# Performance work log

Measured on AMD Instinct MI355X. Metric: run time of the kernel, lower is better.

Reference implementation:

```python
import jax, jax.numpy as jnp
import numpy as np

B, N, E = 16, 1024, 256
H, D = 16, 16            # head_num * qkv_dim == embedding_dim
FF = 2 * E               # ff_size = embedding_dim * 2
EPS = 1e-5


def setup_inputs() -> dict:
    key = jax.random.key(0)
    ks = jax.random.split(key, 12)
    s = lambda fan_in: 1.0 / np.sqrt(fan_in)
    return {
        "x":  jax.random.normal(ks[0], (B, N, E), dtype=jnp.float32),
        # attention projections (nn.Linear, bias=False) stored as [in, out]
        "Wq": jax.random.uniform(ks[1], (E, H * D), jnp.float32, -s(E), s(E)),
        "Wk": jax.random.uniform(ks[2], (E, H * D), jnp.float32, -s(E), s(E)),
        "Wv": jax.random.uniform(ks[3], (E, H * D), jnp.float32, -s(E), s(E)),
        "Wo": jax.random.uniform(ks[4], (H * D, E), jnp.float32, -s(H * D), s(H * D)),
        "bo": jax.random.uniform(ks[5], (E,), jnp.float32, -s(H * D), s(H * D)),
        # InstanceNorm1d affine params
        "gamma1": jnp.ones((E,), jnp.float32),
        "beta1":  jnp.zeros((E,), jnp.float32),
        "gamma2": jnp.ones((E,), jnp.float32),
        "beta2":  jnp.zeros((E,), jnp.float32),
        # SwiGLU FFN: Linear(E, 2*FF) -> SwiGLU -> Linear(FF, E)
        "W1": jax.random.uniform(ks[6], (E, 2 * FF), jnp.float32, -s(E), s(E)),
        "b1": jax.random.uniform(ks[7], (2 * FF,), jnp.float32, -s(E), s(E)),
        "W2": jax.random.uniform(ks[8], (FF, E), jnp.float32, -s(FF), s(FF)),
        "b2": jax.random.uniform(ks[9], (E,), jnp.float32, -s(FF), s(FF)),
    }


def _instance_norm(x, gamma, beta):
    # x: [B, N, E]; normalize over N per (batch, channel), biased variance
    mean = jnp.mean(x, axis=1, keepdims=True)
    var = jnp.mean(jnp.square(x - mean), axis=1, keepdims=True)
    return (x - mean) * jax.lax.rsqrt(var + EPS) * gamma + beta


def reference(x, Wq, Wk, Wv, Wo, bo, gamma1, beta1, gamma2, beta2, W1, b1, W2, b2):
    b, n, e = x.shape
    q = (x @ Wq).reshape(b, n, H, D)
    k = (x @ Wk).reshape(b, n, H, D)
    v = (x @ Wv).reshape(b, n, H, D)
    scores = jnp.einsum("bnhd,bmhd->bhnm", q, k) / np.sqrt(D)   # [B,H,N,N]
    weights = jax.nn.softmax(scores, axis=-1)
    attn = jnp.einsum("bhnm,bmhd->bnhd", weights, v).reshape(b, n, H * D)
    mha = attn @ Wo + bo
    h = _instance_norm(mha + x, gamma1, beta1)
    # SwiGLU FFN: chunk -> (x_part, gate); silu(gate) * x_part
    proj = h @ W1 + b1
    x_part, gate = proj[..., :FF], proj[..., FF:]
    ff = (jax.nn.silu(gate) * x_part) @ W2 + b2
    return _instance_norm(h + ff, gamma2, beta2)
```

## Files before the change

kernel.cpp:

```cpp
#include <hip/hip_runtime.h>
#include <stdint.h>

typedef unsigned short u16;
typedef __bf16 bf16x8 __attribute__((ext_vector_type(8)));
typedef float f32x4 __attribute__((ext_vector_type(4)));

__device__ __forceinline__ float bf2f(u16 v){ return __uint_as_float(((unsigned)v)<<16); }
__device__ __forceinline__ u16 f2bf(float f){
  unsigned u = __float_as_uint(f);
  unsigned r = (u + 0x7FFFu + ((u>>16)&1u)) >> 16;
  return (u16)r;
}
__device__ __forceinline__ float fexp2(float x){
#if __has_builtin(__builtin_amdgcn_exp2f)
  return __builtin_amdgcn_exp2f(x);
#else
  return exp2f(x);
#endif
}

__global__ void prep_kernel(const float* __restrict__ x_, u16* __restrict__ xb,
                            const float* __restrict__ Wq, const float* __restrict__ Wk,
                            const float* __restrict__ Wv, const float* __restrict__ Wo,
                            const float* __restrict__ W1, const float* __restrict__ W2,
                            u16* __restrict__ wqkvT, u16* __restrict__ woT,
                            u16* __restrict__ w1T, u16* __restrict__ w2T)
{
  int bid = blockIdx.x;
  int t = threadIdx.x;
  if (bid >= 640) {
    int idx = ((bid - 640) * 256 + t) * 8;
    float4 a0 = *(const float4*)(x_ + idx);
    float4 a1 = *(const float4*)(x_ + idx + 4);
    union { u16 u[8]; uint4 v; } pk;
    pk.u[0] = f2bf(a0.x); pk.u[1] = f2bf(a0.y); pk.u[2] = f2bf(a0.z); pk.u[3] = f2bf(a0.w);
    pk.u[4] = f2bf(a1.x); pk.u[5] = f2bf(a1.y); pk.u[6] = f2bf(a1.z); pk.u[7] = f2bf(a1.w);
    *(uint4*)(xb + idx) = pk.v;
    return;
  }
  __shared__ u16 tile[32][33];
  const float* in; u16* out; int K, N, t2; bool glu = false;
  if (bid < 64)       { in = Wq; out = wqkvT;           K = 256; N = 256;  t2 = bid; }
  else if (bid < 128) { in = Wk; out = wqkvT + 65536;   K = 256; N = 256;  t2 = bid - 64; }
  else if (bid < 192) { in = Wv; out = wqkvT + 131072;  K = 256; N = 256;  t2 = bid - 128; }
  else if (bid < 256) { in = Wo; out = woT;             K = 256; N = 256;  t2 = bid - 192; }
  else if (bid < 512) { in = W1; out = w1T;             K = 256; N = 1024; t2 = bid - 256; glu = true; }
  else                { in = W2; out = w2T;             K = 512; N = 256;  t2 = bid - 512; }
  int ntn = N >> 5;
  int k0 = (t2 / ntn) * 32, n0 = (t2 % ntn) * 32;
  #pragma unroll
  for (int p = 0; p < 4; ++p) {
    int u = t + p * 256; int r = u >> 5, c = u & 31;
    tile[r][c] = f2bf(in[(size_t)(k0 + r) * N + n0 + c]);
  }
  __syncthreads();
  #pragma unroll
  for (int p = 0; p < 4; ++p) {
    int u = t + p * 256; int r = u >> 5, c = u & 31;
    int q = n0 + r;
    int row = glu ? (q < 512 ? 2 * q : 2 * (q - 512) + 1) : q;
    out[(size_t)row * K + k0 + c] = tile[c][r];
  }
}

enum { MODE_QKV = 0, MODE_Y_RES = 1, MODE_GLU = 2 };

template<int MODE, int RESF32, int STATS>
__launch_bounds__(256, 2)
__global__ void gemm_kernel(const u16* __restrict__ A, const u16* __restrict__ BT,
                            int M, int N, int K,
                            const float* __restrict__ bias, const void* __restrict__ resp,
                            u16* __restrict__ outB,
                            float* __restrict__ ssum, float* __restrict__ ssq)
{
  __shared__ u16 As[128 * 40];
  __shared__ u16 Bs[128 * 40];
  const int t = threadIdx.x;
  const int m0 = blockIdx.x * 128;
  const int n0 = blockIdx.y * 128;
  const int lane = t & 63;
  const int w = t >> 6;
  const int wm = (w >> 1) * 64;
  const int wn = (w & 1) * 64;
  const int fr = lane & 15;
  const int fg = lane >> 4;

  f32x4 acc[4][4];
  #pragma unroll
  for (int i = 0; i < 4; ++i)
    #pragma unroll
    for (int j = 0; j < 4; ++j)
      acc[i][j] = (f32x4){0.f, 0.f, 0.f, 0.f};

  for (int k0 = 0; k0 < K; k0 += 32) {
    __syncthreads();
    #pragma unroll
    for (int p = 0; p < 2; ++p) {
      int u = t + p * 256;
      int row = u >> 2, cb = u & 3;
      float4 va = *(const float4*)(A + (size_t)(m0 + row) * K + k0 + cb * 8);
      *(float4*)(As + row * 40 + cb * 8) = va;
      float4 vb = *(const float4*)(BT + (size_t)(n0 + row) * K + k0 + cb * 8);
      *(float4*)(Bs + row * 40 + cb * 8) = vb;
    }
    __syncthreads();
    bf16x8 af[4], bfr[4];
    #pragma unroll
    for (int i = 0; i < 4; ++i) af[i]  = *(const bf16x8*)(As + (wm + i * 16 + fr) * 40 + fg * 8);
    #pragma unroll
    for (int j = 0; j < 4; ++j) bfr[j] = *(const bf16x8*)(Bs + (wn + j * 16 + fr) * 40 + fg * 8);
    #pragma unroll
    for (int i = 0; i < 4; ++i)
      #pragma unroll
      for (int j = 0; j < 4; ++j)
        acc[i][j] = __builtin_amdgcn_mfma_f32_16x16x32_bf16(af[i], bfr[j], acc[i][j], 0, 0, 0);
  }

  const int bIdx = m0 >> 10;
  #pragma unroll
  for (int j = 0; j < 4; ++j) {
    int col = n0 + wn + j * 16 + fr;
    float bv = 0.f;
    if (MODE == MODE_Y_RES) bv = bias[col];
    if (MODE == MODE_GLU)   bv = bias[(col >> 1) + ((col & 1) << 9)];
    float sj = 0.f, qj = 0.f;
    #pragma unroll
    for (int i = 0; i < 4; ++i) {
      #pragma unroll
      for (int r = 0; r < 4; ++r) {
        int row = m0 + wm + i * 16 + fg * 4 + r;
        float v = acc[i][j][r] + bv;
        if (MODE == MODE_QKV) {
          int which = col >> 8, h = (col >> 4) & 15, d = col & 15;
          int b = row >> 10, ns = row & 1023;
          outB[(size_t)which * 4194304 + (((size_t)(b * 16 + h) * 1024 + ns) * 16 + d)] = f2bf(v);
        } else if (MODE == MODE_Y_RES) {
          size_t idx = (size_t)row * N + col;
          float rv = RESF32 ? ((const float*)resp)[idx] : bf2f(((const u16*)resp)[idx]);
          float y = v + rv;
          outB[idx] = f2bf(y);
          if (STATS) { sj += y; qj += y * y; }
        } else {
          float partner = __shfl_xor(v, 1);
          if ((fr & 1) == 0) {
            float g = partner / (1.f + __expf(-partner));
            outB[(size_t)row * 512 + (col >> 1)] = f2bf(g * v);
          }
        }
      }
    }
    if (STATS) {
      sj += __shfl_xor(sj, 16); sj += __shfl_xor(sj, 32);
      qj += __shfl_xor(qj, 16); qj += __shfl_xor(qj, 32);
      if (fg == 0) {
        atomicAdd(&ssum[bIdx * 256 + col], sj);
        atomicAdd(&ssq[bIdx * 256 + col], qj);
      }
    }
  }
}

#define SCALE_L2 0.360673760222241f

__launch_bounds__(512, 4)
__global__ void attn_kernel(const u16* __restrict__ Q, const u16* __restrict__ Kg,
                            const u16* __restrict__ Vg, u16* __restrict__ attn)
{
  __shared__ u16 Ks[2][128 * 24];
  __shared__ u16 Vt[2][16 * 136];
  __shared__ u16 Pb[8][16 * 40];
  const int t = threadIdx.x;
  const int bh = blockIdx.x & 255;
  const int qg = blockIdx.x >> 8;
  const int b = bh >> 4, h = bh & 15;
  const size_t base = (size_t)bh * 16384;
  const int w = t >> 6, lane = t & 63;
  const int fr = lane & 15, fg = lane >> 4;
  u16* Pw = Pb[w];
  const int q0 = qg * 128 + w * 16;
  const f32x4 zero4 = (f32x4){0.f, 0.f, 0.f, 0.f};

  const int su = (t & 255) >> 1;
  const int sh = t & 1;
  const bool isK = t < 256;
  const int blk = su >> 5, ii = su & 31;
  const int kpos = blk * 32 + ((ii & 1) ? 16 + (ii >> 1) : (ii >> 1));

  bf16x8 qf = {};
  if (fg < 2) {
    union { u16 u[8]; uint4 v; bf16x8 f; } qt;
    qt.v = *(const uint4*)(Q + base + (size_t)(q0 + fr) * 16 + fg * 8);
    #pragma unroll
    for (int j = 0; j < 8; ++j) qt.u[j] = f2bf(bf2f(qt.u[j]) * SCALE_L2);
    qf = qt.f;
  }

  {
    uint4 pre = isK ? *(const uint4*)(Kg + base + (size_t)su * 16 + sh * 8)
                    : *(const uint4*)(Vg + base + (size_t)su * 16 + sh * 8);
    if (isK) {
      *(uint4*)(&Ks[0][kpos * 24 + sh * 8]) = pre;
    } else {
      union { u16 u[8]; uint4 v; } pk; pk.v = pre;
      #pragma unroll
      for (int j = 0; j < 8; ++j) Vt[0][(sh * 8 + j) * 136 + su] = pk.u[j];
    }
  }
  __syncthreads();

  f32x4 acco = zero4;
  float lsum[4] = {0.f, 0.f, 0.f, 0.f};

  for (int c = 0; c < 8; ++c) {
    uint4 nxt;
    if (c < 7) {
      const size_t off = base + (size_t)((c + 1) * 128 + su) * 16 + sh * 8;
      nxt = isK ? *(const uint4*)(Kg + off) : *(const uint4*)(Vg + off);
    }
    const u16* KsC = Ks[c & 1];
    const u16* VtC = Vt[c & 1];
    #pragma unroll
    for (int sub = 0; sub < 4; ++sub) {
      const int kb = sub * 32;
      bf16x8 kf0 = {}, kf1 = {};
      if (fg < 2) {
        kf0 = *(const bf16x8*)(KsC + (kb + fr) * 24 + fg * 8);
        kf1 = *(const bf16x8*)(KsC + (kb + 16 + fr) * 24 + fg * 8);
      }
      f32x4 s0 = __builtin_amdgcn_mfma_f32_16x16x32_bf16(qf, kf0, zero4, 0, 0, 0);
      f32x4 s1 = __builtin_amdgcn_mfma_f32_16x16x32_bf16(qf, kf1, zero4, 0, 0, 0);
      #pragma unroll
      for (int r = 0; r < 4; ++r) {
        float p0 = fexp2(s0[r]);
        float p1 = fexp2(s1[r]);
        lsum[r] += p0 + p1;
        *(unsigned*)(Pw + (fg * 4 + r) * 40 + 2 * fr) =
            __builtin_amdgcn_perm(__float_as_uint(p1), __float_as_uint(p0), 0x07060302u);
      }
      __asm__ volatile("s_waitcnt lgkmcnt(0)" ::: "memory");
      bf16x8 pf = *(const bf16x8*)(Pw + fr * 40 + fg * 8);
      bf16x8 vf = *(const bf16x8*)(VtC + fr * 136 + kb + fg * 8);
      __asm__ volatile("" ::: "memory");
      acco = __builtin_amdgcn_mfma_f32_16x16x32_bf16(pf, vf, acco, 0, 0, 0);
    }
    if (c < 7) {
      if (isK) {
        *(uint4*)(&Ks[(c + 1) & 1][kpos * 24 + sh * 8]) = nxt;
      } else {
        union { u16 u[8]; uint4 v; } pk; pk.v = nxt;
        #pragma unroll
        for (int j = 0; j < 8; ++j) Vt[(c + 1) & 1][(sh * 8 + j) * 136 + su] = pk.u[j];
      }
    }
    __syncthreads();
  }

  #pragma unroll
  for (int r = 0; r < 4; ++r) {
    float l = lsum[r];
    l += __shfl_xor(l, 1); l += __shfl_xor(l, 2);
    l += __shfl_xor(l, 4); l += __shfl_xor(l, 8);
    int row = q0 + fg * 4 + r;
    attn[((size_t)(b * 1024 + row)) * 256 + h * 16 + fr] = f2bf(acco[r] / l);
  }
}

template<int OUTBF16>
__global__ void apply_kernel(const u16* __restrict__ y, const float* __restrict__ ssum,
                             const float* __restrict__ ssq, const float* __restrict__ gamma,
                             const float* __restrict__ beta, void* __restrict__ outp)
{
  int idx = (blockIdx.x * 256 + threadIdx.x) * 4;
  int e = idx & 255;
  int b = idx >> 18;
  union { u16 u[4]; uint2 v; } in;
  in.v = *(const uint2*)(y + idx);
  float ov[4];
  const float inv = 1.f / 1024.f;
  #pragma unroll
  for (int j = 0; j < 4; ++j) {
    int ej = e + j;
    float mean = ssum[b * 256 + ej] * inv;
    float var = ssq[b * 256 + ej] * inv - mean * mean;
    float rstd = rsqrtf(var + 1e-5f);
    ov[j] = (bf2f(in.u[j]) - mean) * rstd * gamma[ej] + beta[ej];
  }
  if (OUTBF16) {
    union { u16 u[4]; uint2 v; } pk;
    #pragma unroll
    for (int j = 0; j < 4; ++j) pk.u[j] = f2bf(ov[j]);
    *(uint2*)((u16*)outp + idx) = pk.v;
  } else {
    *(float4*)((float*)outp + idx) = make_float4(ov[0], ov[1], ov[2], ov[3]);
  }
}

extern "C" void kernel_launch(void* const* d_in, const int* in_sizes, int n_in,
                              void* d_out, int out_size, void* d_ws, size_t ws_size,
                              hipStream_t stream)
{
  const float* x      = (const float*)d_in[0];
  const float* Wq     = (const float*)d_in[1];
  const float* Wk     = (const float*)d_in[2];
  const float* Wv     = (const float*)d_in[3];
  const float* Wo     = (const float*)d_in[4];
  const float* bo     = (const float*)d_in[5];
  const float* gamma1 = (const float*)d_in[6];
  const float* beta1  = (const float*)d_in[7];
  const float* gamma2 = (const float*)d_in[8];
  const float* beta2  = (const float*)d_in[9];
  const float* W1     = (const float*)d_in[10];
  const float* b1     = (const float*)d_in[11];
  const float* W2     = (const float*)d_in[12];
  const float* b2     = (const float*)d_in[13];

  char* ws = (char*)d_ws;
  u16*   WQKVT = (u16*)(ws + 0);
  u16*   WOT   = (u16*)(ws + 393216);
  u16*   W1T   = (u16*)(ws + 524288);
  u16*   W2T   = (u16*)(ws + 1048576);
  float* SS    = (float*)(ws + 1310720);
  float* SSUM1 = SS;
  float* SSQ1  = SS + 4096;
  float* SSUM2 = SS + 8192;
  float* SSQ2  = SS + 12288;
  u16*   xb    = (u16*)(ws + 1376256);
  u16*   Qb    = (u16*)(ws + 9764864);
  u16*   ATTN  = (u16*)(ws + 1376256);
  u16*   Y1    = (u16*)(ws + 9764864);
  u16*   Hf    = (u16*)(ws + 26542080);
  u16*   G     = (u16*)(ws + 34930688);
  u16*   Y2    = (u16*)(ws + 1376256);

  hipMemsetAsync(SS, 0, 65536, stream);
  prep_kernel<<<2688, 256, 0, stream>>>(x, xb, Wq, Wk, Wv, Wo, W1, W2,
                                        WQKVT, WOT, W1T, W2T);

  gemm_kernel<MODE_QKV, 0, 0><<<dim3(128, 6), 256, 0, stream>>>(
      xb, WQKVT, 16384, 768, 256, nullptr, nullptr, Qb, nullptr, nullptr);

  attn_kernel<<<2048, 512, 0, stream>>>(Qb, Qb + 4194304, Qb + 8388608, ATTN);

  gemm_kernel<MODE_Y_RES, 1, 1><<<dim3(128, 2), 256, 0, stream>>>(
      ATTN, WOT, 16384, 256, 256, bo, x, Y1, SSUM1, SSQ1);

  apply_kernel<1><<<4096, 256, 0, stream>>>(Y1, SSUM1, SSQ1, gamma1, beta1, Hf);

  gemm_kernel<MODE_GLU, 0, 0><<<dim3(128, 8), 256, 0, stream>>>(
      Hf, W1T, 16384, 1024, 256, b1, nullptr, G, nullptr, nullptr);

  gemm_kernel<MODE_Y_RES, 0, 1><<<dim3(128, 2), 256, 0, stream>>>(
      G, W2T, 16384, 256, 512, b2, Hf, Y2, SSUM2, SSQ2);

  apply_kernel<0><<<4096, 256, 0, stream>>>(Y2, SSUM2, SSQ2, gamma2, beta2, (float*)d_out);
}
```

Before: 237.7 us.

## Fuse first instance-norm apply into GLU and W2 GEMMs, drop memset

```diff
diff --git a/kernel.cpp b/kernel.cpp
--- a/kernel.cpp
+++ b/kernel.cpp
@@ -24,7 +24,8 @@
                             const float* __restrict__ Wv, const float* __restrict__ Wo,
                             const float* __restrict__ W1, const float* __restrict__ W2,
                             u16* __restrict__ wqkvT, u16* __restrict__ woT,
-                            u16* __restrict__ w1T, u16* __restrict__ w2T)
+                            u16* __restrict__ w1T, u16* __restrict__ w2T,
+                            float* __restrict__ SS)
 {
   int bid = blockIdx.x;
   int t = threadIdx.x;
@@ -38,6 +39,7 @@
     *(uint4*)(xb + idx) = pk.v;
     return;
   }
+  if (bid < 64) SS[bid * 256 + t] = 0.f;
   __shared__ u16 tile[32][33];
   const float* in; u16* out; int K, N, t2; bool glu = false;
   if (bid < 64)       { in = Wq; out = wqkvT;           K = 256; N = 256;  t2 = bid; }
@@ -65,64 +67,111 @@
 
 enum { MODE_QKV = 0, MODE_Y_RES = 1, MODE_GLU = 2 };
 
-template<int MODE, int RESF32, int STATS>
-__launch_bounds__(256, 2)
+template<int MODE, int TN, int RESN, int STATS, int NORMA>
+__launch_bounds__(256, 3)
 __global__ void gemm_kernel(const u16* __restrict__ A, const u16* __restrict__ BT,
                             int M, int N, int K,
-                            const float* __restrict__ bias, const void* __restrict__ resp,
+                            const float* __restrict__ bias, const u16* __restrict__ resp,
                             u16* __restrict__ outB,
-                            float* __restrict__ ssum, float* __restrict__ ssq)
-{
+                            float* __restrict__ ssum, float* __restrict__ ssq,
+                            const float* __restrict__ nsum, const float* __restrict__ nsq,
+                            const float* __restrict__ ngam, const float* __restrict__ nbet)
+{
+  constexpr int NJ = TN / 32;
   __shared__ u16 As[128 * 40];
-  __shared__ u16 Bs[128 * 40];
+  __shared__ u16 Bs[TN * 40];
+  __shared__ float scA[256], sfA[256];
   const int t = threadIdx.x;
   const int m0 = blockIdx.x * 128;
-  const int n0 = blockIdx.y * 128;
+  const int n0 = blockIdx.y * TN;
   const int lane = t & 63;
   const int w = t >> 6;
   const int wm = (w >> 1) * 64;
-  const int wn = (w & 1) * 64;
+  const int wn = (w & 1) * (NJ * 16);
   const int fr = lane & 15;
   const int fg = lane >> 4;
-
-  f32x4 acc[4][4];
+  const int bIdx = m0 >> 10;
+  const float inv1024 = 1.f / 1024.f;
+
+  if (NORMA) {
+    int e = t;
+    float mean = nsum[bIdx * 256 + e] * inv1024;
+    float var = nsq[bIdx * 256 + e] * inv1024 - mean * mean;
+    float rstd = rsqrtf(var + 1e-5f);
+    float sc = rstd * ngam[e];
+    scA[e] = sc;
+    sfA[e] = nbet[e] - mean * sc;
+  }
+
+  f32x4 acc[4][NJ];
   #pragma unroll
   for (int i = 0; i < 4; ++i)
     #pragma unroll
-    for (int j = 0; j < 4; ++j)
+    for (int j = 0; j < NJ; ++j)
       acc[i][j] = (f32x4){0.f, 0.f, 0.f, 0.f};
 
+  constexpr int TOT = (128 + TN) * 4;
   for (int k0 = 0; k0 < K; k0 += 32) {
     __syncthreads();
     #pragma unroll
-    for (int p = 0; p < 2; ++p) {
-      int u = t + p * 256;
-      int row = u >> 2, cb = u & 3;
-      float4 va = *(const float4*)(A + (size_t)(m0 + row) * K + k0 + cb * 8);
-      *(float4*)(As + row * 40 + cb * 8) = va;
-      float4 vb = *(const float4*)(BT + (size_t)(n0 + row) * K + k0 + cb * 8);
-      *(float4*)(Bs + row * 40 + cb * 8) = vb;
+    for (int u = 0; u < TOT / 256; ++u) {
+      int uu = t + u * 256;
+      if (uu < 512) {
+        int row = uu >> 2, cb = uu & 3;
+        if (NORMA) {
+          union { u16 u[8]; uint4 v; } in, o;
+          in.v = *(const uint4*)(A + (size_t)(m0 + row) * K + k0 + cb * 8);
+          const float* scp = scA + k0 + cb * 8;
+          const float* sfp = sfA + k0 + cb * 8;
+          float4 s0 = *(const float4*)scp, s1 = *(const float4*)(scp + 4);
+          float4 f0 = *(const float4*)sfp, f1 = *(const float4*)(sfp + 4);
+          o.u[0] = f2bf(bf2f(in.u[0]) * s0.x + f0.x);
+          o.u[1] = f2bf(bf2f(in.u[1]) * s0.y + f0.y);
+          o.u[2] = f2bf(bf2f(in.u[2]) * s0.z + f0.z);
+          o.u[3] = f2bf(bf2f(in.u[3]) * s0.w + f0.w);
+          o.u[4] = f2bf(bf2f(in.u[4]) * s1.x + f1.x);
+          o.u[5] = f2bf(bf2f(in.u[5]) * s1.y + f1.y);
+          o.u[6] = f2bf(bf2f(in.u[6]) * s1.z + f1.z);
+          o.u[7] = f2bf(bf2f(in.u[7]) * s1.w + f1.w);
+          *(uint4*)(As + row * 40 + cb * 8) = o.v;
+        } else {
+          float4 va = *(const float4*)(A + (size_t)(m0 + row) * K + k0 + cb * 8);
+          *(float4*)(As + row * 40 + cb * 8) = va;
+        }
+      } else {
+        int v2 = uu - 512;
+        int row = v2 >> 2, cb = v2 & 3;
+        float4 vb = *(const float4*)(BT + (size_t)(n0 + row) * K + k0 + cb * 8);
+        *(float4*)(Bs + row * 40 + cb * 8) = vb;
+      }
     }
     __syncthreads();
-    bf16x8 af[4], bfr[4];
+    bf16x8 af[4], bfr[NJ];
     #pragma unroll
     for (int i = 0; i < 4; ++i) af[i]  = *(const bf16x8*)(As + (wm + i * 16 + fr) * 40 + fg * 8);
     #pragma unroll
-    for (int j = 0; j < 4; ++j) bfr[j] = *(const bf16x8*)(Bs + (wn + j * 16 + fr) * 40 + fg * 8);
+    for (int j = 0; j < NJ; ++j) bfr[j] = *(const bf16x8*)(Bs + (wn + j * 16 + fr) * 40 + fg * 8);
     #pragma unroll
     for (int i = 0; i < 4; ++i)
       #pragma unroll
-      for (int j = 0; j < 4; ++j)
+      for (int j = 0; j < NJ; ++j)
         acc[i][j] = __builtin_amdgcn_mfma_f32_16x16x32_bf16(af[i], bfr[j], acc[i][j], 0, 0, 0);
   }
 
-  const int bIdx = m0 >> 10;
-  #pragma unroll
-  for (int j = 0; j < 4; ++j) {
+  #pragma unroll
+  for (int j = 0; j < NJ; ++j) {
     int col = n0 + wn + j * 16 + fr;
     float bv = 0.f;
     if (MODE == MODE_Y_RES) bv = bias[col];
     if (MODE == MODE_GLU)   bv = bias[(col >> 1) + ((col & 1) << 9)];
+    float scj = 0.f, sfj = 0.f;
+    if (RESN == 2) {
+      float mean = nsum[bIdx * 256 + col] * inv1024;
+      float var = nsq[bIdx * 256 + col] * inv1024 - mean * mean;
+      float rstd = rsqrtf(var + 1e-5f);
+      scj = rstd * ngam[col];
+      sfj = nbet[col] - mean * scj;
+    }
     float sj = 0.f, qj = 0.f;
     #pragma unroll
     for (int i = 0; i < 4; ++i) {
@@ -136,7 +185,8 @@
           outB[(size_t)which * 4194304 + (((size_t)(b * 16 + h) * 1024 + ns) * 16 + d)] = f2bf(v);
         } else if (MODE == MODE_Y_RES) {
           size_t idx = (size_t)row * N + col;
-          float rv = RESF32 ? ((const float*)resp)[idx] : bf2f(((const u16*)resp)[idx]);
+          float rv = bf2f(resp[idx]);
+          if (RESN == 2) rv = rv * scj + sfj;
           float y = v + rv;
           outB[idx] = f2bf(y);
           if (STATS) { sj += y; qj += y * y; }
@@ -265,10 +315,9 @@
   }
 }
 
-template<int OUTBF16>
 __global__ void apply_kernel(const u16* __restrict__ y, const float* __restrict__ ssum,
                              const float* __restrict__ ssq, const float* __restrict__ gamma,
-                             const float* __restrict__ beta, void* __restrict__ outp)
+                             const float* __restrict__ beta, float* __restrict__ outp)
 {
   int idx = (blockIdx.x * 256 + threadIdx.x) * 4;
   int e = idx & 255;
@@ -285,14 +334,7 @@
     float rstd = rsqrtf(var + 1e-5f);
     ov[j] = (bf2f(in.u[j]) - mean) * rstd * gamma[ej] + beta[ej];
   }
-  if (OUTBF16) {
-    union { u16 u[4]; uint2 v; } pk;
-    #pragma unroll
-    for (int j = 0; j < 4; ++j) pk.u[j] = f2bf(ov[j]);
-    *(uint2*)((u16*)outp + idx) = pk.v;
-  } else {
-    *(float4*)((float*)outp + idx) = make_float4(ov[0], ov[1], ov[2], ov[3]);
-  }
+  *(float4*)(outp + idx) = make_float4(ov[0], ov[1], ov[2], ov[3]);
 }
 
 extern "C" void kernel_launch(void* const* d_in, const int* in_sizes, int n_in,
@@ -326,31 +368,31 @@
   float* SSQ2  = SS + 12288;
   u16*   xb    = (u16*)(ws + 1376256);
   u16*   Qb    = (u16*)(ws + 9764864);
-  u16*   ATTN  = (u16*)(ws + 1376256);
+  u16*   ATTN  = (u16*)(ws + 34930688);
   u16*   Y1    = (u16*)(ws + 9764864);
-  u16*   Hf    = (u16*)(ws + 26542080);
-  u16*   G     = (u16*)(ws + 34930688);
-  u16*   Y2    = (u16*)(ws + 1376256);
-
-  hipMemsetAsync(SS, 0, 65536, stream);
+  u16*   G     = (u16*)(ws + 18153472);
+  u16*   Y2    = (u16*)(ws + 34930688);
+
   prep_kernel<<<2688, 256, 0, stream>>>(x, xb, Wq, Wk, Wv, Wo, W1, W2,
-                                        WQKVT, WOT, W1T, W2T);
-
-  gemm_kernel<MODE_QKV, 0, 0><<<dim3(128, 6), 256, 0, stream>>>(
-      xb, WQKVT, 16384, 768, 256, nullptr, nullptr, Qb, nullptr, nullptr);
+                                        WQKVT, WOT, W1T, W2T, SS);
+
+  gemm_kernel<MODE_QKV, 128, 0, 0, 0><<<dim3(128, 6), 256, 0, stream>>>(
+      xb, WQKVT, 16384, 768, 256, nullptr, nullptr, Qb,
+      nullptr, nullptr, nullptr, nullptr, nullptr, nullptr);
 
   attn_kernel<<<2048, 512, 0, stream>>>(Qb, Qb + 4194304, Qb + 8388608, ATTN);
 
-  gemm_kernel<MODE_Y_RES, 1, 1><<<dim3(128, 2), 256, 0, stream>>>(
-      ATTN, WOT, 16384, 256, 256, bo, x, Y1, SSUM1, SSQ1);
-
-  apply_kernel<1><<<4096, 256, 0, stream>>>(Y1, SSUM1, SSQ1, gamma1, beta1, Hf);
-
-  gemm_kernel<MODE_GLU, 0, 0><<<dim3(128, 8), 256, 0, stream>>>(
-      Hf, W1T, 16384, 1024, 256, b1, nullptr, G, nullptr, nullptr);
-
-  gemm_kernel<MODE_Y_RES, 0, 1><<<dim3(128, 2), 256, 0, stream>>>(
-      G, W2T, 16384, 256, 512, b2, Hf, Y2, SSUM2, SSQ2);
-
-  apply_kernel<0><<<4096, 256, 0, stream>>>(Y2, SSUM2, SSQ2, gamma2, beta2, (float*)d_out);
-}
+  gemm_kernel<MODE_Y_RES, 64, 1, 1, 0><<<dim3(128, 4), 256, 0, stream>>>(
+      ATTN, WOT, 16384, 256, 256, bo, xb, Y1,
+      SSUM1, SSQ1, nullptr, nullptr, nullptr, nullptr);
+
+  gemm_kernel<MODE_GLU, 128, 0, 0, 1><<<dim3(128, 8), 256, 0, stream>>>(
+      Y1, W1T, 16384, 1024, 256, b1, nullptr, G,
+      nullptr, nullptr, SSUM1, SSQ1, gamma1, beta1);
+
+  gemm_kernel<MODE_Y_RES, 64, 2, 1, 0><<<dim3(128, 4), 256, 0, stream>>>(
+      G, W2T, 16384, 256, 512, b2, Y1, Y2,
+      SSUM2, SSQ2, SSUM1, SSQ1, gamma1, beta1);
+
+  apply_kernel<<<4096, 256, 0, stream>>>(Y2, SSUM2, SSQ2, gamma2, beta2, (float*)d_out);
+}
```

Result: faster. 225.9 us (-4.9%).
